# Kernel tuning notes

Measured on AMD Instinct MI355X. Metric: run time of the kernel, lower is better.

Reference implementation:

```python
import jax, jax.numpy as jnp
import numpy as np

B, D_IN, T, H, OUT = 128, 128, 1024, 512, 2


def setup_inputs() -> dict:
    key = jax.random.key(0)
    ks = jax.random.split(key, 12)
    s = 1.0 / np.sqrt(H)  # torch LSTM/Linear init scale
    u = lambda k, shape: jax.random.uniform(k, shape, jnp.float32, -s, s)
    return {
        "x": jax.random.normal(ks[0], (B, D_IN, T), jnp.float32),
        # layer 0 (input_dim -> H), gate order i,f,g,o stacked along 4H
        "Wih0": u(ks[1], (4 * H, D_IN)),
        "Whh0": u(ks[2], (4 * H, H)),
        "bih0": u(ks[3], (4 * H,)),
        "bhh0": u(ks[4], (4 * H,)),
        # layer 1 (H -> H)
        "Wih1": u(ks[5], (4 * H, H)),
        "Whh1": u(ks[6], (4 * H, H)),
        "bih1": u(ks[7], (4 * H,)),
        "bhh1": u(ks[8], (4 * H,)),
        # linear head
        "fcW": u(ks[9], (OUT, H)),
        "fcb": u(ks[10], (OUT,)),
    }


def _lstm_layer(x_btd, Wih, Whh, bih, bhh):
    """One unidirectional LSTM layer. x_btd: (B,T,D). Returns (hs_bth, h_last)."""
    h_dim = Whh.shape[1]
    b = x_btd.shape[0]
    # precompute input contribution for all timesteps: (T, B, 4H)
    xg = jnp.einsum("btd,gd->tbg", x_btd, Wih) + (bih + bhh)

    def step(carry, xg_t):
        h, c = carry
        gates = xg_t + h @ Whh.T  # (B, 4H)
        i, f, g, o = jnp.split(gates, 4, axis=-1)
        i = jax.nn.sigmoid(i)
        f = jax.nn.sigmoid(f)
        g = jnp.tanh(g)
        o = jax.nn.sigmoid(o)
        c = f * c + i * g
        h = o * jnp.tanh(c)
        return (h, c), h

    h0 = jnp.zeros((b, h_dim), x_btd.dtype)
    c0 = jnp.zeros((b, h_dim), x_btd.dtype)
    (h_last, _), hs = jax.lax.scan(step, (h0, c0), xg)
    return jnp.transpose(hs, (1, 0, 2)), h_last  # (B,T,H), (B,H)


def reference(x, Wih0, Whh0, bih0, bhh0, Wih1, Whh1, bih1, bhh1, fcW, fcb):
    x_btd = jnp.transpose(x, (0, 2, 1))  # (B, T, D_IN), mirrors x.transpose(1,2)
    hs0, _ = _lstm_layer(x_btd, Wih0, Whh0, bih0, bhh0)
    _, h_last = _lstm_layer(hs0, Wih1, Whh1, bih1, bhh1)
    return h_last @ fcW.T + fcb  # fc(hidden[-1]) -> (B, OUT)
```

## Files before the change

### kernel.cpp

```cpp
#include <hip/hip_runtime.h>
#include <hip/hip_fp16.h>


typedef _Float16 half8 __attribute__((ext_vector_type(8)));
typedef float f32x4 __attribute__((ext_vector_type(4)));
typedef unsigned long long u64;
typedef u64 u64x2 __attribute__((ext_vector_type(2)));

#define MFMA16(a, b, c) __builtin_amdgcn_mfma_f32_16x16x32_f16((a), (b), (c), 0, 0, 0)

#define WS_H0_OFF (64 << 10)
#define WS_H1_OFF (576 << 10)
#define WS_XTW_OFF (832 << 10)
#define SYNC_CLAIM 1024
#define SYNC_MODE 1040
#define SYNC_ARRIVE 1056
#define SYNC_FLAG0 1280
#define SYNC_FLAG1 1536

__device__ __forceinline__ float sigf(float x) {
  return __builtin_amdgcn_rcpf(1.f + exp2f(-1.44269504f * x));
}
__device__ __forceinline__ float tanhf_(float x) {
  return 1.f - 2.f * __builtin_amdgcn_rcpf(1.f + exp2f(2.88539008f * x));
}
__device__ __forceinline__ unsigned short f2h(float x) {
  _Float16 h = (_Float16)x;
  unsigned short b;
  __builtin_memcpy(&b, &h, 2);
  return b;
}
__device__ __forceinline__ u64 lda(const u64* p) {
  return __hip_atomic_load(p, __ATOMIC_RELAXED, __HIP_MEMORY_SCOPE_AGENT);
}
__device__ __forceinline__ unsigned lda32(const unsigned* p) {
  return __hip_atomic_load(p, __ATOMIC_RELAXED, __HIP_MEMORY_SCOPE_AGENT);
}

__device__ __forceinline__ void cvt_split(const f32x4& a, const f32x4& b,
                                          half8& hi, half8& lo) {
#pragma unroll
  for (int i = 0; i < 4; ++i) {
    float w0 = a[i], w1 = b[i];
    _Float16 h0 = (_Float16)w0, h1 = (_Float16)w1;
    hi[i] = h0;
    hi[i + 4] = h1;
    lo[i] = (_Float16)((w0 - (float)h0) * 2048.0f);
    lo[i + 4] = (_Float16)((w1 - (float)h1) * 2048.0f);
  }
}
__device__ __forceinline__ half8 hscale(half8 v) {
  half8 r;
#pragma unroll
  for (int i = 0; i < 8; ++i) r[i] = v[i] * (_Float16)4.8828125e-4f;
  return r;
}

__global__ void __launch_bounds__(256) prep_kernel(const float* __restrict__ x,
                                                   _Float16* __restrict__ xTw,
                                                   unsigned* __restrict__ sync,
                                                   float* __restrict__ out) {
  const int bid = blockIdx.x;
  const int c = bid >> 4, b16 = bid & 15;
  const int tid = threadIdx.x;
  if (bid == 0) {
#pragma unroll
    for (int i = 0; i < 16; ++i) sync[i * 256 + tid] = 0;
    out[tid] = 0.f;
  }
  const int d = tid & 127, th = tid >> 7;
  const float* src = x + ((size_t)(c * 16 + b16) * 128 + d) * 1024 + th * 16;
  _Float16* dst = xTw + ((size_t)c * 32 + th * 16) * (16 * 128) + b16 * 128 + d;
#pragma unroll
  for (int i = 0; i < 16; ++i) dst[(size_t)i * (16 * 128)] = (_Float16)src[i];
}

__global__ void __launch_bounds__(256, 2) lstm_scan(
    const float* __restrict__ Whh0, const float* __restrict__ bih0,
    const float* __restrict__ bhh0, const float* __restrict__ Wih1,
    const float* __restrict__ Whh1, const float* __restrict__ bih1,
    const float* __restrict__ bhh1, const float* __restrict__ fcW,
    const float* __restrict__ fcb, const float* __restrict__ Wih0,
    const float* __restrict__ x, unsigned* __restrict__ sync,
    unsigned short* __restrict__ exch, _Float16* __restrict__ xTw,
    float* __restrict__ out) {
  __shared__ __align__(16) _Float16 hbuf[3][16][4][16][8];
  __shared__ unsigned s_bcast[2];
  __shared__ unsigned wdone[4];

  const int tid = threadIdx.x;
  const int wave = tid >> 6;
  const int lane = tid & 63;
  const int q = lane >> 4;
  const int bb = lane & 15;

  unsigned xcc;
  asm("s_getreg_b32 %0, hwreg(HW_REG_XCC_ID)" : "=s"(xcc));
  xcc &= 7;
  unsigned* claim = sync + SYNC_CLAIM;
  unsigned* modew = sync + SYNC_MODE;
  unsigned* arrive = sync + SYNC_ARRIVE;
  if (tid < 4) wdone[tid] = 0;
  if (tid == 0) {
    unsigned idx = __hip_atomic_fetch_add(claim + xcc, 1u, __ATOMIC_RELAXED,
                                          __HIP_MEMORY_SCOPE_AGENT);
    unsigned ord = __hip_atomic_fetch_add(arrive, 1u + (idx >> 31),
                                          __ATOMIC_RELAXED,
                                          __HIP_MEMORY_SCOPE_AGENT);
    if (ord == 511u) {
      unsigned ok = 1;
#pragma unroll
      for (int i = 0; i < 8; ++i)
        ok &= (__hip_atomic_load(claim + i, __ATOMIC_RELAXED,
                                 __HIP_MEMORY_SCOPE_AGENT) == 64u);
      __hip_atomic_store(modew, ok ? 2u : 1u, __ATOMIC_RELAXED,
                         __HIP_MEMORY_SCOPE_AGENT);
    }
    unsigned mv = 0;
    int guard = 0;
    for (;;) {
      mv = __hip_atomic_load(modew, __ATOMIC_RELAXED, __HIP_MEMORY_SCOPE_AGENT);
      if (mv != 0u) break;
      if (++guard > (1 << 18)) { mv = 1u; break; }
    }
    s_bcast[0] = mv;
    s_bcast[1] = idx;
  }
  __syncthreads();
  const bool loc = (s_bcast[0] == 2u);
  const unsigned idx = s_bcast[1];
  bool roleL1;
  int c, wg;
  if (loc) {
    c = (int)xcc;
    roleL1 = idx >= 32u;
    wg = roleL1 ? (int)idx - 32 : (int)idx;
  } else {
    const int b = blockIdx.x;
    roleL1 = b >= 256;
    const int b2 = roleL1 ? b - 256 : b;
    c = b2 >> 5;
    wg = b2 & 31;
  }

  const int wcl = wg * 4 + wave;
  const int chbase = wcl * 4;
  const int m = lane & 15;
  const int arow = (m & 3) * 512 + chbase + (m >> 2);
  unsigned short* xtw16 = (unsigned short*)xTw;
  unsigned short* exch1 = exch + ((512 << 10) >> 1);
  const int ch = chbase + q;
  const int hoff = (((ch >> 5) * 4 + ((ch >> 3) & 3)) * 16) * 8 + (ch & 7) +
                   bb * 8;

  unsigned* flag0 = sync + SYNC_FLAG0 + c * 32;
  unsigned* flag1 = sync + SYNC_FLAG1 + c * 32;
  const unsigned* f0q = flag0 + (lane & 31);
  const unsigned* f1q = flag1 + (lane & 31);
  const int T = 1024;


  if (!roleL1) {
    half8 fW0[16], fW0lo[16], fX[4], fXlo[4];
    {
      const float* p0 = Whh0 + (size_t)arow * 512 + q * 8;
#pragma unroll
      for (int kt = 0; kt < 16; ++kt) {
        f32x4 a0 = *(const f32x4*)(p0 + kt * 32),
              b0 = *(const f32x4*)(p0 + kt * 32 + 4);
        cvt_split(a0, b0, fW0[kt], fW0lo[kt]);
      }
      const float* p3 = Wih0 + (size_t)arow * 128 + q * 8;
#pragma unroll
      for (int kt = 0; kt < 4; ++kt) {
        f32x4 a3 = *(const f32x4*)(p3 + kt * 32),
              b3 = *(const f32x4*)(p3 + kt * 32 + 4);
        cvt_split(a3, b3, fX[kt], fXlo[kt]);
      }
    }
    float b0v[4];
#pragma unroll
    for (int g = 0; g < 4; ++g) {
      int rrow = g * 512 + chbase + q;
      b0v[g] = bih0[rrow] + bhh0[rrow];
    }

    float c0 = 0.f;
    for (int r = 0; r < T; ++r) {
      const bool doref = (wave == 2 && r < 992 && (r & 3) == 0);

      f32x4 xv4;
      int sw = 0, rw = 0, xb = 0, xd = 0;
      if (doref) {
        const int wnext = (r >> 5) + 1;
        sw = wnext % 3; rw = r & 31;
        xb = wg >> 1; xd = (wg & 1) * 64 + lane;
        xv4 = *(const f32x4*)(x + ((size_t)(c * 16 + xb) * 128 + xd) * 1024 +
                              wnext * 32 + rw);
      }

      half8 xf[4];
      {
        const int s = (r >> 5) % 3, tau = r & 31;
        const u64* xp = (const u64*)xtw16 +
                        (((size_t)(s * 8 + c) * 32 + tau) * 16 + bb) * 32;
        if (loc) {
#pragma unroll
          for (int kt = 0; kt < 4; ++kt)
            xf[kt] =
                __builtin_bit_cast(half8, *(const u64x2*)(xp + kt * 8 + q * 2));
        } else {
#pragma unroll
          for (int kt = 0; kt < 4; ++kt) {
            u64x2 t2;
            t2.x = lda(xp + kt * 8 + q * 2);
            t2.y = lda(xp + kt * 8 + q * 2 + 1);
            xf[kt] = __builtin_bit_cast(half8, t2);
          }
        }
      }

      f32x4 accX = {b0v[0], b0v[1], b0v[2], b0v[3]};
#pragma unroll
      for (int kt = 0; kt < 4; ++kt) {
        accX = MFMA16(fX[kt], xf[kt], accX);
        accX = MFMA16(fXlo[kt], hscale(xf[kt]), accX);
      }

      if (r > 0) {
        int guard = 0;
        for (;;) {
          unsigned f0 = lda32(f0q), f1 = lda32(f1q);
          bool ok = ((int)f0 >= r) && ((int)f1 >= r - 3);
          if (__ballot(ok) == ~0ull) break;
          if (++guard > 4096) break;
        }
        asm volatile("" ::: "memory");
        if (loc) {
          const u64x2* src =
              (const u64x2*)exch + ((size_t)((r - 1) & 3) * 8 + c) * 1024 + tid;
          u64x2 v[4];
#pragma unroll
          for (int i = 0; i < 4; ++i) v[i] = src[i * 256];
          u64x2* dst = (u64x2*)hbuf[0] + tid;
#pragma unroll
          for (int i = 0; i < 4; ++i) dst[i * 256] = v[i];
        } else {
          const u64* src =
              (const u64*)exch + ((size_t)((r - 1) & 3) * 8 + c) * 2048 + tid;
          u64 v[8];
#pragma unroll
          for (int i = 0; i < 8; ++i) v[i] = lda(src + i * 256);
          u64* dst = (u64*)hbuf[0] + tid;
#pragma unroll
          for (int i = 0; i < 8; ++i) dst[i * 256] = v[i];
        }
      }
      __syncthreads();

      f32x4 a0 = {0.f, 0.f, 0.f, 0.f};
      f32x4 a0b = a0, a0l = a0, a0bl = a0;
      if (r > 0) {
#pragma unroll
        for (int kt = 0; kt < 8; ++kt) {
          half8 hA = *(const half8*)(&hbuf[0][kt][q][bb][0]);
          half8 hB = *(const half8*)(&hbuf[0][kt + 8][q][bb][0]);
          a0 = MFMA16(fW0[kt], hA, a0);
          a0b = MFMA16(fW0[kt + 8], hB, a0b);
          a0l = MFMA16(fW0lo[kt], hscale(hA), a0l);
          a0bl = MFMA16(fW0lo[kt + 8], hscale(hB), a0bl);
        }
      }
      f32x4 g0 = accX + ((a0 + a0b) + (a0l + a0bl));
      float gi = sigf(g0.x), gf = sigf(g0.y), gg = tanhf_(g0.z),
            go = sigf(g0.w);
      c0 = gf * c0 + gi * gg;
      float h0v = go * tanhf_(c0);
      size_t hidx = ((size_t)(r & 3) * 8 + c) * 8192 + hoff;
      if (loc)
        exch[hidx] = f2h(h0v);
      else
        __hip_atomic_store(exch + hidx, f2h(h0v), __ATOMIC_RELAXED,
                           __HIP_MEMORY_SCOPE_AGENT);

      asm volatile("s_waitcnt vmcnt(0)" ::: "memory");
      __hip_atomic_store(&wdone[wave], (unsigned)(r + 1), __ATOMIC_RELAXED,
                         __HIP_MEMORY_SCOPE_WORKGROUP);
      if (wave == 0) {
        int guard = 0;
        for (;;) {
          unsigned w = __hip_atomic_load(&wdone[lane & 3], __ATOMIC_RELAXED,
                                         __HIP_MEMORY_SCOPE_WORKGROUP);
          if (__ballot(w >= (unsigned)(r + 1)) == ~0ull) break;
          if (++guard > 8192) break;
        }
        if (lane == 0) {
          if (loc)
            __hip_atomic_store(flag0 + wg, (unsigned)(r + 1), __ATOMIC_RELAXED,
                               __HIP_MEMORY_SCOPE_WORKGROUP);
          else
            __hip_atomic_store(flag0 + wg, (unsigned)(r + 1), __ATOMIC_RELAXED,
                               __HIP_MEMORY_SCOPE_AGENT);
        }
      }

      if (doref) {
#pragma unroll
        for (int j = 0; j < 4; ++j) {
          size_t xidx =
              (((size_t)(sw * 8 + c) * 32 + rw + j) * 16 + xb) * 128 + xd;
          if (loc)
            xtw16[xidx] = f2h(xv4[j]);
          else
            __hip_atomic_store(xtw16 + xidx, f2h(xv4[j]), __ATOMIC_RELAXED,
                               __HIP_MEMORY_SCOPE_AGENT);
        }
      }
    }
  } else {
    half8 fW1i[16], fW1ilo[16], fW1h[16];
    {
      const float* p1 = Wih1 + (size_t)arow * 512 + q * 8;
      const float* p2 = Whh1 + (size_t)arow * 512 + q * 8;
#pragma unroll
      for (int kt = 0; kt < 16; ++kt) {
        f32x4 a1 = *(const f32x4*)(p1 + kt * 32),
              b1 = *(const f32x4*)(p1 + kt * 32 + 4);
        cvt_split(a1, b1, fW1i[kt], fW1ilo[kt]);
        f32x4 a2 = *(const f32x4*)(p2 + kt * 32),
              b2 = *(const f32x4*)(p2 + kt * 32 + 4);
        half8 dummy;
        cvt_split(a2, b2, fW1h[kt], dummy);
      }
    }
    float b1v[4];
#pragma unroll
    for (int g = 0; g < 4; ++g) {
      int rrow = g * 512 + chbase + q;
      b1v[g] = bih1[rrow] + bhh1[rrow];
    }
    const float fcw0 = fcW[ch], fcw1 = fcW[512 + ch];

    float c1 = 0.f;
    f32x4 a1 = {b1v[0], b1v[1], b1v[2], b1v[3]};
    f32x4 a1b = {0.f, 0.f, 0.f, 0.f};

    {
      int guard = 0;
      for (;;) {
        unsigned f0 = lda32(f0q);
        bool ok = ((int)f0 >= 1);
        if (__ballot(ok) == ~0ull) break;
        if (++guard > 8192) break;
      }
      asm volatile("" ::: "memory");
      if (loc) {
        const u64x2* src = (const u64x2*)exch + (size_t)c * 1024 + tid;
        u64x2 v[4];
#pragma unroll
        for (int i = 0; i < 4; ++i) v[i] = src[i * 256];
        u64x2* dst = (u64x2*)hbuf[1] + tid;
#pragma unroll
        for (int i = 0; i < 4; ++i) dst[i * 256] = v[i];
      } else {
        const u64* src = (const u64*)exch + (size_t)c * 2048 + tid;
        u64 v[8];
#pragma unroll
        for (int i = 0; i < 8; ++i) v[i] = lda(src + i * 256);
        u64* dst = (u64*)hbuf[1] + tid;
#pragma unroll
        for (int i = 0; i < 8; ++i) dst[i * 256] = v[i];
      }
      __syncthreads();
#pragma unroll
      for (int kt = 0; kt < 8; ++kt) {
        half8 hA = *(const half8*)(&hbuf[1][kt][q][bb][0]);
        half8 hB = *(const half8*)(&hbuf[1][kt + 8][q][bb][0]);
        a1 = MFMA16(fW1i[kt], hA, a1);
        a1b = MFMA16(fW1i[kt + 8], hB, a1b);
        a1 = MFMA16(fW1ilo[kt], hscale(hA), a1);
        a1b = MFMA16(fW1ilo[kt + 8], hscale(hB), a1b);
      }
    }

    for (int t = 0; t < T; ++t) {
      if (t > 0) {
        int guard = 0;
        for (;;) {
          unsigned f1 = lda32(f1q);
          bool ok = ((int)f1 >= t);
          if (__ballot(ok) == ~0ull) break;
          if (++guard > 4096) break;
        }
        asm volatile("" ::: "memory");
        if (loc) {
          const u64x2* src = (const u64x2*)exch1 +
                             ((size_t)((t - 1) & 1) * 8 + c) * 1024 + tid;
          u64x2 v[4];
#pragma unroll
          for (int i = 0; i < 4; ++i) v[i] = src[i * 256];
          u64x2* dst = (u64x2*)hbuf[0] + tid;
#pragma unroll
          for (int i = 0; i < 4; ++i) dst[i * 256] = v[i];
        } else {
          const u64* src =
              (const u64*)exch1 + ((size_t)((t - 1) & 1) * 8 + c) * 2048 + tid;
          u64 v[8];
#pragma unroll
          for (int i = 0; i < 8; ++i) v[i] = lda(src + i * 256);
          u64* dst = (u64*)hbuf[0] + tid;
#pragma unroll
          for (int i = 0; i < 8; ++i) dst[i * 256] = v[i];
        }
      }
      __syncthreads();

      f32x4 a1c = {0.f, 0.f, 0.f, 0.f};
      f32x4 a1d = a1c;
      if (t > 0) {
#pragma unroll
        for (int kt = 0; kt < 8; ++kt) {
          half8 hC = *(const half8*)(&hbuf[0][kt][q][bb][0]);
          half8 hD = *(const half8*)(&hbuf[0][kt + 8][q][bb][0]);
          a1c = MFMA16(fW1h[kt], hC, a1c);
          a1d = MFMA16(fW1h[kt + 8], hD, a1d);
        }
      }
      f32x4 g1 = (a1 + a1b) + (a1c + a1d);
      float gi = sigf(g1.x), gf = sigf(g1.y), gg = tanhf_(g1.z),
            go = sigf(g1.w);
      c1 = gf * c1 + gi * gg;
      float h1v = go * tanhf_(c1);

      if (t == T - 1) {
        float s0 = h1v * fcw0, s1 = h1v * fcw1;
        s0 += __shfl_xor(s0, 16); s0 += __shfl_xor(s0, 32);
        s1 += __shfl_xor(s1, 16); s1 += __shfl_xor(s1, 32);
        if (q == 0) {
          atomicAdd(out + (size_t)(c * 16 + bb) * 2 + 0, s0);
          atomicAdd(out + (size_t)(c * 16 + bb) * 2 + 1, s1);
        }
        if (wcl == 0 && lane < 32)
          atomicAdd(out + (size_t)(c * 16 + (lane & 15)) * 2 + (lane >> 4),
                    fcb[lane >> 4]);
      } else {
        size_t hidx = ((size_t)(t & 1) * 8 + c) * 8192 + hoff;
        if (loc)
          exch1[hidx] = f2h(h1v);
        else
          __hip_atomic_store(exch1 + hidx, f2h(h1v), __ATOMIC_RELAXED,
                             __HIP_MEMORY_SCOPE_AGENT);
      }

      asm volatile("s_waitcnt vmcnt(0)" ::: "memory");
      __hip_atomic_store(&wdone[wave], (unsigned)(t + 1), __ATOMIC_RELAXED,
                         __HIP_MEMORY_SCOPE_WORKGROUP);
      if (wave == 0) {
        int guard = 0;
        for (;;) {
          unsigned w = __hip_atomic_load(&wdone[lane & 3], __ATOMIC_RELAXED,
                                         __HIP_MEMORY_SCOPE_WORKGROUP);
          if (__ballot(w >= (unsigned)(t + 1)) == ~0ull) break;
          if (++guard > 8192) break;
        }
        if (lane == 0) {
          if (loc)
            __hip_atomic_store(flag1 + wg, (unsigned)(t + 1), __ATOMIC_RELAXED,
                               __HIP_MEMORY_SCOPE_WORKGROUP);
          else
            __hip_atomic_store(flag1 + wg, (unsigned)(t + 1), __ATOMIC_RELAXED,
                               __HIP_MEMORY_SCOPE_AGENT);
        }
      }

      if (t < T - 1) {
        int guard = 0;
        for (;;) {
          unsigned f0 = lda32(f0q);
          bool ok = ((int)f0 >= t + 2);
          if (__ballot(ok) == ~0ull) break;
          if (++guard > 4096) break;
        }
        asm volatile("" ::: "memory");
        const int buf = 1 + ((t + 1) & 1);
        if (loc) {
          const u64x2* src = (const u64x2*)exch +
                             ((size_t)((t + 1) & 3) * 8 + c) * 1024 + tid;
          u64x2 v[4];
#pragma unroll
          for (int i = 0; i < 4; ++i) v[i] = src[i * 256];
          u64x2* dst = (u64x2*)hbuf[buf] + tid;
#pragma unroll
          for (int i = 0; i < 4; ++i) dst[i * 256] = v[i];
        } else {
          const u64* src =
              (const u64*)exch + ((size_t)((t + 1) & 3) * 8 + c) * 2048 + tid;
          u64 v[8];
#pragma unroll
          for (int i = 0; i < 8; ++i) v[i] = lda(src + i * 256);
          u64* dst = (u64*)hbuf[buf] + tid;
#pragma unroll
          for (int i = 0; i < 8; ++i) dst[i * 256] = v[i];
        }
        __syncthreads();
        a1 = {b1v[0], b1v[1], b1v[2], b1v[3]};
        a1b = {0.f, 0.f, 0.f, 0.f};
#pragma unroll
        for (int kt = 0; kt < 8; ++kt) {
          half8 hA = *(const half8*)(&hbuf[buf][kt][q][bb][0]);
          half8 hB = *(const half8*)(&hbuf[buf][kt + 8][q][bb][0]);
          a1 = MFMA16(fW1i[kt], hA, a1);
          a1b = MFMA16(fW1i[kt + 8], hB, a1b);
          a1 = MFMA16(fW1ilo[kt], hscale(hA), a1);
          a1b = MFMA16(fW1ilo[kt + 8], hscale(hB), a1b);
        }
      }
    }
  }
}

extern "C" void kernel_launch(void* const* d_in, const int* in_sizes, int n_in,
                              void* d_out, int out_size, void* d_ws,
                              size_t ws_size, hipStream_t stream) {
  const float* x = (const float*)d_in[0];
  const float* Wih0 = (const float*)d_in[1];
  const float* Whh0 = (const float*)d_in[2];
  const float* bih0 = (const float*)d_in[3];
  const float* bhh0 = (const float*)d_in[4];
  const float* Wih1 = (const float*)d_in[5];
  const float* Whh1 = (const float*)d_in[6];
  const float* bih1 = (const float*)d_in[7];
  const float* bhh1 = (const float*)d_in[8];
  const float* fcW = (const float*)d_in[9];
  const float* fcb = (const float*)d_in[10];

  char* ws = (char*)d_ws;
  unsigned* sync = (unsigned*)ws;
  unsigned short* exch = (unsigned short*)(ws + WS_H0_OFF);
  _Float16* xTw = (_Float16*)(ws + WS_XTW_OFF);
  float* out = (float*)d_out;

  prep_kernel<<<dim3(128), dim3(256), 0, stream>>>(x, xTw, sync, out);
  lstm_scan<<<dim3(512), dim3(256), 0, stream>>>(Whh0, bih0, bhh0, Wih1, Whh1,
                                                 bih1, bhh1, fcW, fcb, Wih0, x,
                                                 sync, exch, xTw, out);
}
```

Baseline: 3.174 ms.

## Stage h in LDS and publish via one coalesced wave store per step

Each thread now writes its fp16 hidden value into a small shared buffer, and a __syncthreads replaces the per-wave wdone flag spin. Wave 0 then writes the whole 512-byte workgroup slice to the global exchange buffer with 64-bit stores before raising the flag. This removes 256 scattered 2-byte global stores per step and the LDS polling loop. Nontemporal loads are also added for reading x. The cost is a full block barrier on the per-step critical path and a serialized store-then-flag sequence in wave 0.

Result: faster. 3.007 ms (-5.3%).

```diff
diff --git a/kernel.cpp b/kernel.cpp
--- a/kernel.cpp
+++ b/kernel.cpp
@@ -36,6 +36,12 @@
 __device__ __forceinline__ unsigned lda32(const unsigned* p) {
   return __hip_atomic_load(p, __ATOMIC_RELAXED, __HIP_MEMORY_SCOPE_AGENT);
 }
+__device__ __forceinline__ f32x4 ldnt4(const float* p) {
+  u64x2 t;
+  t.x = __builtin_nontemporal_load((const u64*)p);
+  t.y = __builtin_nontemporal_load((const u64*)p + 1);
+  return __builtin_bit_cast(f32x4, t);
+}
 
 __device__ __forceinline__ void cvt_split(const f32x4& a, const f32x4& b,
                                           half8& hi, half8& lo) {
@@ -72,7 +78,8 @@
   const float* src = x + ((size_t)(c * 16 + b16) * 128 + d) * 1024 + th * 16;
   _Float16* dst = xTw + ((size_t)c * 32 + th * 16) * (16 * 128) + b16 * 128 + d;
 #pragma unroll
-  for (int i = 0; i < 16; ++i) dst[(size_t)i * (16 * 128)] = (_Float16)src[i];
+  for (int i = 0; i < 16; ++i)
+    dst[(size_t)i * (16 * 128)] = (_Float16)__builtin_nontemporal_load(src + i);
 }
 
 __global__ void __launch_bounds__(256, 2) lstm_scan(
@@ -85,8 +92,8 @@
     unsigned short* __restrict__ exch, _Float16* __restrict__ xTw,
     float* __restrict__ out) {
   __shared__ __align__(16) _Float16 hbuf[3][16][4][16][8];
+  __shared__ __align__(16) unsigned short pbuf[256];
   __shared__ unsigned s_bcast[2];
-  __shared__ unsigned wdone[4];
 
   const int tid = threadIdx.x;
   const int wave = tid >> 6;
@@ -100,7 +107,6 @@
   unsigned* claim = sync + SYNC_CLAIM;
   unsigned* modew = sync + SYNC_MODE;
   unsigned* arrive = sync + SYNC_ARRIVE;
-  if (tid < 4) wdone[tid] = 0;
   if (tid == 0) {
     unsigned idx = __hip_atomic_fetch_add(claim + xcc, 1u, __ATOMIC_RELAXED,
                                           __HIP_MEMORY_SCOPE_AGENT);
@@ -150,15 +156,14 @@
   unsigned short* xtw16 = (unsigned short*)xTw;
   unsigned short* exch1 = exch + ((512 << 10) >> 1);
   const int ch = chbase + q;
-  const int hoff = (((ch >> 5) * 4 + ((ch >> 3) & 3)) * 16) * 8 + (ch & 7) +
-                   bb * 8;
+  const int lch = wave * 4 + q;
+  const int ppos = (lch >> 3) * 128 + bb * 8 + (lch & 7);
 
   unsigned* flag0 = sync + SYNC_FLAG0 + c * 32;
   unsigned* flag1 = sync + SYNC_FLAG1 + c * 32;
   const unsigned* f0q = flag0 + (lane & 31);
   const unsigned* f1q = flag1 + (lane & 31);
   const int T = 1024;
-
 
   if (!roleL1) {
     half8 fW0[16], fW0lo[16], fX[4], fXlo[4];
@@ -195,8 +200,8 @@
         const int wnext = (r >> 5) + 1;
         sw = wnext % 3; rw = r & 31;
         xb = wg >> 1; xd = (wg & 1) * 64 + lane;
-        xv4 = *(const f32x4*)(x + ((size_t)(c * 16 + xb) * 128 + xd) * 1024 +
-                              wnext * 32 + rw);
+        xv4 = ldnt4(x + ((size_t)(c * 16 + xb) * 128 + xd) * 1024 +
+                    wnext * 32 + rw);
       }
 
       half8 xf[4];
@@ -276,24 +281,19 @@
             go = sigf(g0.w);
       c0 = gf * c0 + gi * gg;
       float h0v = go * tanhf_(c0);
-      size_t hidx = ((size_t)(r & 3) * 8 + c) * 8192 + hoff;
-      if (loc)
-        exch[hidx] = f2h(h0v);
-      else
-        __hip_atomic_store(exch + hidx, f2h(h0v), __ATOMIC_RELAXED,
-                           __HIP_MEMORY_SCOPE_AGENT);
-
-      asm volatile("s_waitcnt vmcnt(0)" ::: "memory");
-      __hip_atomic_store(&wdone[wave], (unsigned)(r + 1), __ATOMIC_RELAXED,
-                         __HIP_MEMORY_SCOPE_WORKGROUP);
+
+      pbuf[ppos] = f2h(h0v);
+      __syncthreads();
       if (wave == 0) {
-        int guard = 0;
-        for (;;) {
-          unsigned w = __hip_atomic_load(&wdone[lane & 3], __ATOMIC_RELAXED,
-                                         __HIP_MEMORY_SCOPE_WORKGROUP);
-          if (__ballot(w >= (unsigned)(r + 1)) == ~0ull) break;
-          if (++guard > 8192) break;
-        }
+        u64 v = ((const u64*)pbuf)[lane];
+        u64* dst =
+            (u64*)(exch + ((size_t)(r & 3) * 8 + c) * 8192 + wg * 256) + lane;
+        if (loc)
+          *dst = v;
+        else
+          __hip_atomic_store(dst, v, __ATOMIC_RELAXED,
+                             __HIP_MEMORY_SCOPE_AGENT);
+        asm volatile("s_waitcnt vmcnt(0)" ::: "memory");
         if (lane == 0) {
           if (loc)
             __hip_atomic_store(flag0 + wg, (unsigned)(r + 1), __ATOMIC_RELAXED,
@@ -315,6 +315,7 @@
             __hip_atomic_store(xtw16 + xidx, f2h(xv4[j]), __ATOMIC_RELAXED,
                                __HIP_MEMORY_SCOPE_AGENT);
         }
+        asm volatile("s_waitcnt vmcnt(0)" ::: "memory");
       }
     }
   } else {
@@ -443,33 +444,30 @@
         if (wcl == 0 && lane < 32)
           atomicAdd(out + (size_t)(c * 16 + (lane & 15)) * 2 + (lane >> 4),
                     fcb[lane >> 4]);
+        __syncthreads();
       } else {
-        size_t hidx = ((size_t)(t & 1) * 8 + c) * 8192 + hoff;
-        if (loc)
-          exch1[hidx] = f2h(h1v);
-        else
-          __hip_atomic_store(exch1 + hidx, f2h(h1v), __ATOMIC_RELAXED,
-                             __HIP_MEMORY_SCOPE_AGENT);
-      }
-
-      asm volatile("s_waitcnt vmcnt(0)" ::: "memory");
-      __hip_atomic_store(&wdone[wave], (unsigned)(t + 1), __ATOMIC_RELAXED,
-                         __HIP_MEMORY_SCOPE_WORKGROUP);
-      if (wave == 0) {
-        int guard = 0;
-        for (;;) {
-          unsigned w = __hip_atomic_load(&wdone[lane & 3], __ATOMIC_RELAXED,
-                                         __HIP_MEMORY_SCOPE_WORKGROUP);
-          if (__ballot(w >= (unsigned)(t + 1)) == ~0ull) break;
-          if (++guard > 8192) break;
-        }
-        if (lane == 0) {
+        pbuf[ppos] = f2h(h1v);
+        __syncthreads();
+        if (wave == 0) {
+          u64 v = ((const u64*)pbuf)[lane];
+          u64* dst =
+              (u64*)(exch1 + ((size_t)(t & 1) * 8 + c) * 8192 + wg * 256) +
+              lane;
           if (loc)
-            __hip_atomic_store(flag1 + wg, (unsigned)(t + 1), __ATOMIC_RELAXED,
-                               __HIP_MEMORY_SCOPE_WORKGROUP);
+            *dst = v;
           else
-            __hip_atomic_store(flag1 + wg, (unsigned)(t + 1), __ATOMIC_RELAXED,
+            __hip_atomic_store(dst, v, __ATOMIC_RELAXED,
                                __HIP_MEMORY_SCOPE_AGENT);
+          asm volatile("s_waitcnt vmcnt(0)" ::: "memory");
+          if (lane == 0) {
+            if (loc)
+              __hip_atomic_store(flag1 + wg, (unsigned)(t + 1),
+                                 __ATOMIC_RELAXED,
+                                 __HIP_MEMORY_SCOPE_WORKGROUP);
+            else
+              __hip_atomic_store(flag1 + wg, (unsigned)(t + 1),
+                                 __ATOMIC_RELAXED, __HIP_MEMORY_SCOPE_AGENT);
+          }
         }
       }
 
```
